# Kernel tuning notes

Measured on AMD Instinct MI355X. Metric: run time of the kernel, lower is better.

Reference implementation:

```python
import jax, jax.numpy as jnp
import numpy as np

B, H, N, D = 8, 12, 1024, 64
SCALE = 1.0 / float(np.sqrt(D))  # 0.125; torch forward default is 1.0 but 1/sqrt(d) is the production value
EPS = 1e-06


def setup_inputs() -> dict:
    key = jax.random.key(0)
    kq, kk, kv = jax.random.split(key, 3)
    q = jax.random.normal(kq, (B, H, N, D), dtype=jnp.float32)
    k = jax.random.normal(kk, (B, H, N, D), dtype=jnp.float32)
    v = jax.random.normal(kv, (B, H, N, D), dtype=jnp.float32)
    # Parameter init per L2Q.__init__: alpha=0.125, beta=0.5, gamma=1/n_tokens
    alpha = jnp.full((H, 1, 1), 0.125, dtype=jnp.float32)
    beta = jnp.full((H, 1, 1), 0.5, dtype=jnp.float32)
    gamma = jnp.full((H, 1, 1), 1.0 / N, dtype=jnp.float32)
    return {"q": q, "k": k, "v": v, "alpha": alpha, "beta": beta, "gamma": gamma}


def reference(q, k, v, alpha, beta, gamma):
    # logits: (B, H, N, N)
    logits = jnp.einsum("bhnd,bhmd->bhnm", q, k) * SCALE
    # per-head quadratic polynomial, then ReLU; params (H,1,1) broadcast over (B,H,N,N)
    attn = jax.nn.relu(alpha * logits * logits + beta * logits + gamma)
    attn = attn / (jnp.sum(attn, axis=-1, keepdims=True) + EPS)
    return jnp.einsum("bhnm,bhmd->bhnd", attn, v)
```

## Files before the change

### kernel.cpp

```cpp
#include <hip/hip_runtime.h>
#include <hip/hip_bf16.h>

typedef __attribute__((ext_vector_type(8))) short bf16x8;
typedef __attribute__((ext_vector_type(4))) float f32x4;
typedef __attribute__((ext_vector_type(16))) float f32x16;

#define MFMA16(a, b, c) __builtin_amdgcn_mfma_f32_16x16x32_bf16(a, b, c, 0, 0, 0)
#define MFMA32(a, b, c) __builtin_amdgcn_mfma_f32_32x32x16_bf16(a, b, c, 0, 0, 0)

static constexpr int kH = 12;
static constexpr int kN = 1024;
static constexpr int kD = 64;
static constexpr int kBH = 96;
static constexpr int kND = kN * kD;
static constexpr float kScale = 0.125f;
static constexpr float kEps = 1e-6f;
static constexpr long kTensorElems = (long)kBH * kND;
static constexpr long kWsNeeded = 2 * kTensorElems * 2;

__device__ __forceinline__ unsigned bfbits(float x) {
    union { __hip_bfloat16 h; unsigned short u; } c;
    c.h = __float2bfloat16(x);
    return (unsigned)c.u;
}
__device__ __forceinline__ unsigned pack2_rne(float a, float b) {
    return bfbits(a) | (bfbits(b) << 16);
}
__device__ __forceinline__ unsigned pack2_rhu(float lo, float hi) {
    unsigned a = __builtin_bit_cast(unsigned, lo) + 0x8000u;
    unsigned b = __builtin_bit_cast(unsigned, hi) + 0x8000u;
    return __builtin_amdgcn_perm(b, a, 0x07060302u);
}
__device__ __forceinline__ void gl_lds16(const void* g, void* l) {
    __builtin_amdgcn_global_load_lds(
        (const __attribute__((address_space(1))) void*)g,
        (__attribute__((address_space(3))) void*)l, 16, 0, 0);
}

__global__ __launch_bounds__(256, 2) void prep(
    const float* __restrict__ k, const float* __restrict__ v,
    unsigned* __restrict__ kbf, unsigned* __restrict__ vtb)
{
    static constexpr int TS = 68;
    __shared__ float T32[64 * TS];
    const int bid = blockIdx.x;
    const int bh = bid >> 4, nt = bid & 15;
    const int t = threadIdx.x;

    const float* kp = k + (long)bh * kND + (long)nt * 64 * kD;
    unsigned* ko = kbf + ((long)bh * kND + (long)nt * 64 * kD) / 2;
#pragma unroll
    for (int r = 0; r < 4; ++r) {
        const int f4 = t + 256 * r;
        const float4 f = ((const float4*)kp)[f4];
        uint2 u;
        u.x = pack2_rne(f.x, f.y);
        u.y = pack2_rne(f.z, f.w);
        *(uint2*)&ko[f4 * 2] = u;
    }

    const float* vp = v + (long)bh * kND + (long)nt * 64 * kD;
#pragma unroll
    for (int r = 0; r < 4; ++r) {
        const int f4 = t + 256 * r;
        const int n = f4 >> 4, d4 = f4 & 15;
        const float4 f = *(const float4*)(vp + (long)n * kD + 4 * d4);
        *(float4*)&T32[n * TS + 4 * d4] = f;
    }
    __syncthreads();
    const int d = t >> 2, c = t & 3;
    unsigned u[8];
#pragma unroll
    for (int j = 0; j < 8; ++j) {
        const int key = c * 16 + 2 * j;
        u[j] = pack2_rne(T32[key * TS + d], T32[(key + 1) * TS + d]);
    }
    unsigned* dst = vtb + (long)bh * (kND / 2) + (long)d * (kN / 2) + nt * 32 + c * 8;
    *(uint4*)(dst)     = *(uint4*)&u[0];
    *(uint4*)(dst + 4) = *(uint4*)&u[4];
}

__global__ __launch_bounds__(256, 3) void l2q_main(
    const float* __restrict__ q,
    const unsigned short* __restrict__ kbf, const unsigned short* __restrict__ vtbf,
    const float* __restrict__ alpha, const float* __restrict__ beta, const float* __restrict__ gamma,
    float* __restrict__ out)
{
    __shared__ __align__(16) unsigned Ks[2][2048];
    __shared__ __align__(16) unsigned Vs[2][2048];

    const int bid  = blockIdx.x;
    const int xcd  = bid & 7;
    const int sIdx = bid >> 3;
    const int bh   = xcd * 12 + (sIdx % 12);
    const int qt   = sIdx / 12;
    const int h    = bh % kH;
    const int t    = threadIdx.x;
    const int wave = t >> 6;
    const int lane = t & 63;
    const int l31  = lane & 31;
    const int hh   = lane >> 5;

    const float al = alpha[h] * (kScale * kScale);
    const float be = beta[h] * kScale;
    const float ga = gamma[h];

    const float* qp = q + (long)bh * kND;
    const unsigned short* kp = kbf + (long)bh * kND;
    const unsigned short* vp = vtbf + (long)bh * kND;

    bf16x8 qbF[4];
    {
        const int qrow = qt * 128 + wave * 32 + l31;
        const float* qsrc = qp + (long)qrow * kD;
#pragma unroll
        for (int s = 0; s < 4; ++s) {
            const float4 f0 = *(const float4*)(qsrc + s * 16 + hh * 8);
            const float4 f1 = *(const float4*)(qsrc + s * 16 + hh * 8 + 4);
            uint4 u;
            u.x = pack2_rne(f0.x, f0.y);
            u.y = pack2_rne(f0.z, f0.w);
            u.z = pack2_rne(f1.x, f1.y);
            u.w = pack2_rne(f1.z, f1.w);
            qbF[s] = __builtin_bit_cast(bf16x8, u);
        }
    }

    f32x16 oacc[2];
#pragma unroll
    for (int db = 0; db < 2; ++db)
#pragma unroll
        for (int r = 0; r < 16; ++r)
            oacc[db][r] = 0.f;
    float dacc[4] = {0.f, 0.f, 0.f, 0.f};

    const int srow8 = lane >> 3;
    const int g8    = lane & 7;
    auto stageKV = [&](int buf, int tile) {
        const int k0 = tile * 64;
#pragma unroll
        for (int c = 0; c < 2; ++c) {
            const int r = (c * 4 + wave) * 8 + srow8;
            gl_lds16(kp + (long)(k0 + r) * kD + (g8 ^ srow8) * 8, &Ks[buf][(c * 4 + wave) * 256]);
            gl_lds16(vp + (long)r * kN + k0 + (g8 ^ srow8) * 8, &Vs[buf][(c * 4 + wave) * 256]);
        }
    };

    stageKV(0, 0);

    for (int tile = 0; tile < 16; ++tile) {
        const int buf = tile & 1;
        __syncthreads();
        if (tile + 1 < 16) stageKV(buf ^ 1, tile + 1);

        const unsigned* Kb = Ks[buf];
        const unsigned* Vb = Vs[buf];

        f32x16 st[2];
#pragma unroll
        for (int kb = 0; kb < 2; ++kb)
#pragma unroll
            for (int r = 0; r < 16; ++r)
                st[kb][r] = 0.f;
#pragma unroll
        for (int s = 0; s < 4; ++s) {
            const int g = (s << 1) | hh;
#pragma unroll
            for (int kb = 0; kb < 2; ++kb) {
                const int row = kb * 32 + l31;
                bf16x8 ka = *(const bf16x8*)&Kb[row * 32 + ((g ^ (row & 7)) << 2)];
                st[kb] = MFMA32(ka, qbF[s], st[kb]);
            }
        }

        unsigned u[2][8];
#pragma unroll
        for (int kb = 0; kb < 2; ++kb) {
#pragma unroll
            for (int p = 0; p < 8; ++p) {
                const float s0 = st[kb][2 * p], s1 = st[kb][2 * p + 1];
                const float w0 = fmaxf(fmaf(fmaf(al, s0, be), s0, ga), 0.f);
                const float w1 = fmaxf(fmaf(fmaf(al, s1, be), s1, ga), 0.f);
                dacc[p & 3] += w0 + w1;
                u[kb][p] = pack2_rhu(w0, w1);
            }
        }

        bf16x8 pa[4];
#pragma unroll
        for (int s = 0; s < 4; ++s) {
            const int kb = s >> 1;
            const int b = (s & 1) * 4;
            const unsigned snd0 = hh ? u[kb][b + 0] : u[kb][b + 2];
            const unsigned snd1 = hh ? u[kb][b + 1] : u[kb][b + 3];
            const unsigned r0 = (unsigned)__shfl_xor((int)snd0, 32);
            const unsigned r1 = (unsigned)__shfl_xor((int)snd1, 32);
            uint4 fr;
            fr.x = hh ? r0 : u[kb][b + 0];
            fr.y = hh ? r1 : u[kb][b + 1];
            fr.z = hh ? u[kb][b + 2] : r0;
            fr.w = hh ? u[kb][b + 3] : r1;
            pa[s] = __builtin_bit_cast(bf16x8, fr);
        }

#pragma unroll
        for (int db = 0; db < 2; ++db) {
            const int row = db * 32 + l31;
            const int rb = row * 32;
            const int rsw = row & 7;
#pragma unroll
            for (int s = 0; s < 4; ++s) {
                bf16x8 vb = *(const bf16x8*)&Vb[rb + ((((s << 1) | hh) ^ rsw) << 2)];
                oacc[db] = MFMA32(pa[s], vb, oacc[db]);
            }
        }
    }

    float d = (dacc[0] + dacc[1]) + (dacc[2] + dacc[3]);
    d += __shfl_xor(d, 32);
    const float inv = 1.0f / (d + kEps);

    const long obase = (long)bh * kND;
    const int rowbase = qt * 128 + wave * 32;
#pragma unroll
    for (int r = 0; r < 16; ++r) {
        const int row32 = (r & 3) + 8 * (r >> 2) + 4 * hh;
        const float iv = __shfl(inv, row32);
        float* o = out + obase + (long)(rowbase + row32) * kD + l31;
        o[0]  = oacc[0][r] * iv;
        o[32] = oacc[1][r] * iv;
    }
}

static constexpr int KSU = 36;
static constexpr int VSU = 36;
static constexpr int PSU = 36;

__global__ __launch_bounds__(256, 3) void l2q_attn_fb(
    const float* __restrict__ q, const float* __restrict__ k, const float* __restrict__ v,
    const float* __restrict__ alpha, const float* __restrict__ beta, const float* __restrict__ gamma,
    float* __restrict__ out)
{
    __shared__ __align__(16) unsigned KsU[64 * KSU];
    __shared__ __align__(16) unsigned VtU[64 * VSU];
    __shared__ __align__(16) unsigned PU[128 * PSU];

    const int bid  = blockIdx.x;
    const int bh   = bid >> 3;
    const int qt   = bid & 7;
    const int h    = bh % kH;
    const int t    = threadIdx.x;
    const int wave = t >> 6;
    const int lane = t & 63;
    const int quad = lane >> 4;
    const int l15  = lane & 15;

    const float al = alpha[h], be = beta[h], ga = gamma[h];

    const long base = (long)bh * kN * kD;
    const float* qp = q + base;
    const float* kp = k + base;
    const float* vp = v + base;

    bf16x8 qa[2][2];
#pragma unroll
    for (int rb = 0; rb < 2; ++rb) {
        const int row = qt * 128 + wave * 32 + rb * 16 + l15;
#pragma unroll
        for (int kc = 0; kc < 2; ++kc) {
            const float* src = qp + (long)row * kD + kc * 32 + quad * 8;
            const float4 f0 = *(const float4*)(src);
            const float4 f1 = *(const float4*)(src + 4);
            uint4 u;
            u.x = pack2_rne(f0.x, f0.y);
            u.y = pack2_rne(f0.z, f0.w);
            u.z = pack2_rne(f1.x, f1.y);
            u.w = pack2_rne(f1.z, f1.w);
            qa[rb][kc] = __builtin_bit_cast(bf16x8, u);
        }
    }

    f32x4 oacc[2][4];
#pragma unroll
    for (int rb = 0; rb < 2; ++rb)
#pragma unroll
        for (int db = 0; db < 4; ++db)
            oacc[rb][db] = (f32x4){0.f, 0.f, 0.f, 0.f};

    float dsum[2][4] = {{0.f, 0.f, 0.f, 0.f}, {0.f, 0.f, 0.f, 0.f}};
    unsigned* Pw = &PU[wave * 32 * PSU];

    for (int tile = 0; tile < 16; ++tile) {
        __syncthreads();
        const int k0 = tile * 64;
#pragma unroll
        for (int r = 0; r < 4; ++r) {
            const int f4 = t + 256 * r;
            const int n = f4 >> 4, d4 = f4 & 15;
            const float4 kg = *(const float4*)(kp + (long)(k0 + n) * kD + 4 * d4);
            uint2 pk;
            pk.x = pack2_rne(kg.x, kg.y);
            pk.y = pack2_rne(kg.z, kg.w);
            *(uint2*)&KsU[n * KSU + 2 * d4] = pk;
        }
#pragma unroll
        for (int r = 0; r < 2; ++r) {
            const int u = t + 256 * r;
            const int key2 = u & 31, d4 = u >> 5;
            const float* s0 = vp + (long)(k0 + 2 * key2) * kD + 4 * d4;
            const float4 va = *(const float4*)(s0);
            const float4 vb = *(const float4*)(s0 + kD);
            VtU[(4 * d4 + 0) * VSU + key2] = pack2_rne(va.x, vb.x);
            VtU[(4 * d4 + 1) * VSU + key2] = pack2_rne(va.y, vb.y);
            VtU[(4 * d4 + 2) * VSU + key2] = pack2_rne(va.z, vb.z);
            VtU[(4 * d4 + 3) * VSU + key2] = pack2_rne(va.w, vb.w);
        }
        __syncthreads();

        f32x4 s[2][4];
#pragma unroll
        for (int rb = 0; rb < 2; ++rb)
#pragma unroll
            for (int nb = 0; nb < 4; ++nb)
                s[rb][nb] = (f32x4){0.f, 0.f, 0.f, 0.f};
#pragma unroll
        for (int nb = 0; nb < 4; ++nb) {
            bf16x8 kb0 = *(const bf16x8*)&KsU[(nb * 16 + l15) * KSU + 4 * quad];
            bf16x8 kb1 = *(const bf16x8*)&KsU[(nb * 16 + l15) * KSU + 16 + 4 * quad];
#pragma unroll
            for (int rb = 0; rb < 2; ++rb) {
                s[rb][nb] = MFMA16(qa[rb][0], kb0, s[rb][nb]);
                s[rb][nb] = MFMA16(qa[rb][1], kb1, s[rb][nb]);
            }
        }

        const bool ev = (lane & 1) == 0;
#pragma unroll
        for (int rb = 0; rb < 2; ++rb) {
#pragma unroll
            for (int nb = 0; nb < 4; ++nb) {
                float w0, w1, w2, w3;
                {
                    float l0 = s[rb][nb][0] * kScale;
                    float l1 = s[rb][nb][1] * kScale;
                    float l2 = s[rb][nb][2] * kScale;
                    float l3 = s[rb][nb][3] * kScale;
                    w0 = fmaxf(fmaf(fmaf(al, l0, be), l0, ga), 0.f);
                    w1 = fmaxf(fmaf(fmaf(al, l1, be), l1, ga), 0.f);
                    w2 = fmaxf(fmaf(fmaf(al, l2, be), l2, ga), 0.f);
                    w3 = fmaxf(fmaf(fmaf(al, l3, be), l3, ga), 0.f);
                }
                dsum[rb][0] += w0; dsum[rb][1] += w1;
                dsum[rb][2] += w2; dsum[rb][3] += w3;

                const float o0 = __shfl_xor(w0, 1);
                const float o1 = __shfl_xor(w1, 1);
                const float o2 = __shfl_xor(w2, 1);
                const float o3 = __shfl_xor(w3, 1);
                const unsigned pa = ev ? pack2_rne(w0, o0) : pack2_rne(o2, w2);
                const unsigned pb = ev ? pack2_rne(w1, o1) : pack2_rne(o3, w3);
                const int r0 = ev ? 0 : 2;
                const int cu = (16 * nb + (l15 & ~1)) >> 1;
                const int rowb = rb * 16 + quad * 4 + r0;
                Pw[rowb * PSU + cu] = pa;
                Pw[(rowb + 1) * PSU + cu] = pb;
            }
        }

        bf16x8 pf[2][2];
#pragma unroll
        for (int rb = 0; rb < 2; ++rb)
#pragma unroll
            for (int kc = 0; kc < 2; ++kc)
                pf[rb][kc] = *(const bf16x8*)&Pw[(rb * 16 + l15) * PSU + 16 * kc + 4 * quad];
#pragma unroll
        for (int db = 0; db < 4; ++db) {
            bf16x8 vf0 = *(const bf16x8*)&VtU[(db * 16 + l15) * VSU + 4 * quad];
            bf16x8 vf1 = *(const bf16x8*)&VtU[(db * 16 + l15) * VSU + 16 + 4 * quad];
#pragma unroll
            for (int rb = 0; rb < 2; ++rb) {
                oacc[rb][db] = MFMA16(pf[rb][0], vf0, oacc[rb][db]);
                oacc[rb][db] = MFMA16(pf[rb][1], vf1, oacc[rb][db]);
            }
        }
    }

#pragma unroll
    for (int rb = 0; rb < 2; ++rb)
#pragma unroll
        for (int i = 0; i < 4; ++i) {
            float d = dsum[rb][i];
            d += __shfl_xor(d, 1);
            d += __shfl_xor(d, 2);
            d += __shfl_xor(d, 4);
            d += __shfl_xor(d, 8);
            dsum[rb][i] = 1.0f / (d + kEps);
        }

#pragma unroll
    for (int rb = 0; rb < 2; ++rb)
#pragma unroll
        for (int db = 0; db < 4; ++db)
#pragma unroll
            for (int i = 0; i < 4; ++i) {
                const int row = qt * 128 + wave * 32 + rb * 16 + quad * 4 + i;
                out[base + (long)row * kD + db * 16 + l15] = oacc[rb][db][i] * dsum[rb][i];
            }
}

extern "C" void kernel_launch(void* const* d_in, const int* in_sizes, int n_in,
                              void* d_out, int out_size, void* d_ws, size_t ws_size,
                              hipStream_t stream) {
    const float* q     = (const float*)d_in[0];
    const float* k     = (const float*)d_in[1];
    const float* v     = (const float*)d_in[2];
    const float* alpha = (const float*)d_in[3];
    const float* beta  = (const float*)d_in[4];
    const float* gamma = (const float*)d_in[5];
    float* out = (float*)d_out;

    if (ws_size < (size_t)kWsNeeded) {
        l2q_attn_fb<<<dim3(768), dim3(256), 0, stream>>>(q, k, v, alpha, beta, gamma, out);
        return;
    }

    unsigned* kbf = (unsigned*)d_ws;
    unsigned* vtb = kbf + kTensorElems / 2;

    prep<<<dim3(1536), dim3(256), 0, stream>>>(k, v, kbf, vtb);
    l2q_main<<<dim3(768), dim3(256), 0, stream>>>(
        q, (const unsigned short*)kbf, (const unsigned short*)vtb,
        alpha, beta, gamma, out);
}
```

Before: 151.0 us.

## Permute V-transpose key layout to drop cross-lane shuffles in PV MFMA

The V-transpose pre-pass now writes the bf16 key pairs in a permuted order, so the key assignment in the V^T operand matches the per-lane layout of the score accumulator. The main loop can then feed the packed attention weights straight into the PV MFMA, removing the __shfl_xor exchanges and the selects that rebuilt the A fragments. V fragments are also loaded from LDS before the polynomial step so those reads can overlap with ALU work. The layout change and the removed shuffles must agree exactly for the result to stay correct, and the early loads keep eight more bf16x8 registers live, which could hurt occupancy.

Measured after the change: 146.4 us. 3.0% less time.

```diff
diff --git a/kernel.cpp b/kernel.cpp
--- a/kernel.cpp
+++ b/kernel.cpp
@@ -76,8 +76,11 @@
         u[j] = pack2_rne(T32[key * TS + d], T32[(key + 1) * TS + d]);
     }
     unsigned* dst = vtb + (long)bh * (kND / 2) + (long)d * (kN / 2) + nt * 32 + c * 8;
-    *(uint4*)(dst)     = *(uint4*)&u[0];
-    *(uint4*)(dst + 4) = *(uint4*)&u[4];
+    uint4 A, B;
+    A.x = u[0]; A.y = u[1]; A.z = u[4]; A.w = u[5];
+    B.x = u[2]; B.y = u[3]; B.z = u[6]; B.w = u[7];
+    *(uint4*)(dst)     = A;
+    *(uint4*)(dst + 4) = B;
 }
 
 __global__ __launch_bounds__(256, 3) void l2q_main(
@@ -173,6 +176,17 @@
             }
         }
 
+        bf16x8 vfr[2][4];
+#pragma unroll
+        for (int db = 0; db < 2; ++db) {
+            const int row = db * 32 + l31;
+            const int rb = row * 32;
+            const int rsw = row & 7;
+#pragma unroll
+            for (int s = 0; s < 4; ++s)
+                vfr[db][s] = *(const bf16x8*)&Vb[rb + ((((s << 1) | hh) ^ rsw) << 2)];
+        }
+
         unsigned u[2][8];
 #pragma unroll
         for (int kb = 0; kb < 2; ++kb) {
@@ -186,33 +200,17 @@
             }
         }
 
-        bf16x8 pa[4];
 #pragma unroll
         for (int s = 0; s < 4; ++s) {
-            const int kb = s >> 1;
-            const int b = (s & 1) * 4;
-            const unsigned snd0 = hh ? u[kb][b + 0] : u[kb][b + 2];
-            const unsigned snd1 = hh ? u[kb][b + 1] : u[kb][b + 3];
-            const unsigned r0 = (unsigned)__shfl_xor((int)snd0, 32);
-            const unsigned r1 = (unsigned)__shfl_xor((int)snd1, 32);
             uint4 fr;
-            fr.x = hh ? r0 : u[kb][b + 0];
-            fr.y = hh ? r1 : u[kb][b + 1];
-            fr.z = hh ? u[kb][b + 2] : r0;
-            fr.w = hh ? u[kb][b + 3] : r1;
-            pa[s] = __builtin_bit_cast(bf16x8, fr);
-        }
-
-#pragma unroll
-        for (int db = 0; db < 2; ++db) {
-            const int row = db * 32 + l31;
-            const int rb = row * 32;
-            const int rsw = row & 7;
-#pragma unroll
-            for (int s = 0; s < 4; ++s) {
-                bf16x8 vb = *(const bf16x8*)&Vb[rb + ((((s << 1) | hh) ^ rsw) << 2)];
-                oacc[db] = MFMA32(pa[s], vb, oacc[db]);
-            }
+            const int kb = s >> 1, b = (s & 1) * 4;
+            fr.x = u[kb][b + 0];
+            fr.y = u[kb][b + 1];
+            fr.z = u[kb][b + 2];
+            fr.w = u[kb][b + 3];
+            const bf16x8 pa = __builtin_bit_cast(bf16x8, fr);
+            oacc[0] = MFMA32(pa, vfr[0][s], oacc[0]);
+            oacc[1] = MFMA32(pa, vfr[1][s], oacc[1]);
         }
     }
 
```
